# Kernel optimization log

Measured on AMD Instinct MI355X. Metric: run time of the kernel, lower is better.

## Reference

```python
import jax, jax.numpy as jnp
import numpy as np

MARGIN = 0.3


def setup_inputs() -> dict:
    key = jax.random.key(0)
    k1, k2 = jax.random.split(key)
    inputs = jax.random.normal(k1, (8192, 128), dtype=jnp.float32)
    targets = jax.random.randint(k2, (8192,), 0, 512, dtype=jnp.int64)
    return {"inputs": inputs, "targets": targets}


def reference(inputs, targets):
    # inputs: [n, d], targets: [n]
    sq = jnp.sum(inputs * inputs, axis=1)  # [n]
    # dist[i,j] = ||x_i||^2 + ||x_j||^2 - 2 x_i . x_j
    dist = sq[:, None] + sq[None, :] - 2.0 * (inputs @ inputs.T)
    dist = jnp.sqrt(jnp.clip(dist, 1e-12, None))  # [n, n]
    mask = targets[:, None] == targets[None, :]  # True where same label
    # batch-hard mining: hardest positive (max) and hardest negative (min) per row.
    # Diagonal is always True, so every row has at least one positive.
    dist_ap = jnp.max(jnp.where(mask, dist, -jnp.inf), axis=1)  # [n]
    dist_an = jnp.min(jnp.where(mask, jnp.inf, dist), axis=1)  # [n]
    # MarginRankingLoss with y=1: mean(max(0, margin - (dist_an - dist_ap)))
    loss = jnp.mean(jnp.maximum(0.0, MARGIN - (dist_an - dist_ap)))
    prec = jnp.mean((dist_an > dist_ap).astype(jnp.float32))
    return loss, prec
```

## Files before the change

kernel.cpp:

```cpp
#include <hip/hip_runtime.h>
#include <hip/hip_bf16.h>
#include <math.h>

#define N 8192
#define D 128
#define MARGIN 0.3f

#define NSTRIP 64
#define CPS 8
#define TPC 16
#define GRID_MAIN (NSTRIP * CPS)

typedef float f32x4 __attribute__((ext_vector_type(4)));
typedef short bf16x8 __attribute__((ext_vector_type(8)));
typedef unsigned short u16x8 __attribute__((ext_vector_type(8)));

#define AS1 __attribute__((address_space(1)))
#define AS3 __attribute__((address_space(3)))

__device__ inline void gload_lds16(const void* g, void* l) {
    __builtin_amdgcn_global_load_lds((AS1 void*)(void*)(g), (AS3 void*)(l), 16, 0, 0);
}

__device__ inline unsigned short f2bf(float f) {
    unsigned u = __float_as_uint(f);
    unsigned r = (u + 0x7FFFu + ((u >> 16) & 1u)) >> 16;
    return (unsigned short)r;
}

__global__ __launch_bounds__(256) void convert_kernel(const float* __restrict__ X,
                                                      unsigned short* __restrict__ Xb,
                                                      float* __restrict__ sq,
                                                      unsigned* __restrict__ ap2,
                                                      unsigned* __restrict__ an2) {
    int tid = threadIdx.x;
    int row = blockIdx.x * 16 + (tid >> 4);
    int l = tid & 15;
    const float4* p = reinterpret_cast<const float4*>(X + (size_t)row * D + l * 8);
    float4 u = p[0];
    float4 v = p[1];
    float s = u.x*u.x + u.y*u.y + u.z*u.z + u.w*u.w
            + v.x*v.x + v.y*v.y + v.z*v.z + v.w*v.w;
    u16x8 o;
    o[0] = f2bf(u.x); o[1] = f2bf(u.y); o[2] = f2bf(u.z); o[3] = f2bf(u.w);
    o[4] = f2bf(v.x); o[5] = f2bf(v.y); o[6] = f2bf(v.z); o[7] = f2bf(v.w);
    *reinterpret_cast<u16x8*>(Xb + (size_t)row * D + l * 8) = o;
    #pragma unroll
    for (int off = 8; off >= 1; off >>= 1) s += __shfl_xor(s, off);
    if (l == 0) {
        sq[row] = s;
        ap2[row] = 0u;
        an2[row] = 0x7F7F7F7Fu;
    }
}

__global__ __launch_bounds__(512, 4) void triplet_main(
        const unsigned short* __restrict__ Xb,
        const int* __restrict__ lbl,
        const float* __restrict__ sq,
        unsigned* __restrict__ ap2,
        unsigned* __restrict__ an2) {
    __shared__ unsigned short Bs[2][64 * D];
    unsigned short* BsL = &Bs[0][0];

    const int bi = blockIdx.x >> 3;
    const int c  = blockIdx.x & 7;
    const int jt0 = c * TPC;
    const int i0 = bi * 128;

    const int tid = threadIdx.x;
    const int w = tid >> 6;
    const int lane = tid & 63;
    const int wr = w >> 1;
    const int wc = w & 1;
    const int quad = lane >> 4;
    const int lx = lane & 15;

    #pragma unroll
    for (int t = 0; t < 4; ++t) {
        int rbase = w * 16 + t * 4;
        int r = rbase + quad;
        int gc = lx ^ (r & 7);
        gload_lds16(Xb + (size_t)(i0 + r) * D + gc * 8, BsL + rbase * D);
    }

    int lbl_i[8];
    #pragma unroll
    for (int tr = 0; tr < 2; ++tr)
        #pragma unroll
        for (int v = 0; v < 4; ++v)
            lbl_i[tr * 4 + v] = lbl[i0 + wr * 32 + tr * 16 + quad * 4 + v];

    __syncthreads();

    bf16x8 af_r[2][4];
    #pragma unroll
    for (int tr = 0; tr < 2; ++tr) {
        int rA = wr * 32 + tr * 16 + lx;
        #pragma unroll
        for (int ks = 0; ks < 4; ++ks) {
            int sc = (ks * 4 + quad) ^ (lx & 7);
            af_r[tr][ks] = *reinterpret_cast<const bf16x8*>(&BsL[rA * D + sc * 8]);
        }
    }
    __syncthreads();

    #pragma unroll
    for (int t = 0; t < 2; ++t) {
        int rbase = w * 8 + t * 4;
        int r = rbase + quad;
        int gc = lx ^ (r & 7);
        gload_lds16(Xb + (size_t)(jt0 * 64 + r) * D + gc * 8, BsL + rbase * D);
    }

    unsigned vb[2];
    #pragma unroll
    for (int tc = 0; tc < 2; ++tc) {
        int rB = wc * 32 + tc * 16 + lx;
        vb[tc] = (unsigned)(rB * 256 + ((lx & 4) << 4) + ((quad ^ (lx & 3)) << 4));
    }

    float m_ap[8], m_an[8];
    #pragma unroll
    for (int q = 0; q < 8; ++q) { m_ap[q] = -INFINITY; m_an[q] = INFINITY; }
    const f32x4 z4 = {0.f, 0.f, 0.f, 0.f};

    __syncthreads();

    #pragma unroll 2
    for (int tt = 0; tt < TPC; ++tt) {
        const int jj = jt0 + tt;
        const int cur = tt & 1;
        const char* bsb = (const char*)BsL + cur * (64 * D * 2);

        float sqj[2]; int lblj[2];
        #pragma unroll
        for (int tc = 0; tc < 2; ++tc) {
            int jc = jj * 64 + wc * 32 + tc * 16 + lx;
            sqj[tc] = sq[jc];
            lblj[tc] = lbl[jc];
        }

        if (tt + 1 < TPC) {
            unsigned short* nb = BsL + (cur ^ 1) * (64 * D);
            int jn = jj + 1;
            #pragma unroll
            for (int t = 0; t < 2; ++t) {
                int rbase = w * 8 + t * 4;
                int r = rbase + quad;
                int gc = lx ^ (r & 7);
                gload_lds16(Xb + (size_t)(jn * 64 + r) * D + gc * 8, nb + rbase * D);
            }
        }

        f32x4 acc[2][2];
        {
            bf16x8 bf0[2];
            #pragma unroll
            for (int tc = 0; tc < 2; ++tc)
                bf0[tc] = *reinterpret_cast<const bf16x8*>(bsb + (vb[tc] ^ 0u));
            #pragma unroll
            for (int tr = 0; tr < 2; ++tr)
                #pragma unroll
                for (int tc = 0; tc < 2; ++tc)
                    acc[tr][tc] = __builtin_amdgcn_mfma_f32_16x16x32_bf16(
                        af_r[tr][0], bf0[tc], z4, 0, 0, 0);
        }
        #pragma unroll
        for (int ks = 1; ks < 4; ++ks) {
            bf16x8 bf[2];
            #pragma unroll
            for (int tc = 0; tc < 2; ++tc)
                bf[tc] = *reinterpret_cast<const bf16x8*>(bsb + (vb[tc] ^ (unsigned)(ks << 6)));
            #pragma unroll
            for (int tr = 0; tr < 2; ++tr)
                #pragma unroll
                for (int tc = 0; tc < 2; ++tc)
                    acc[tr][tc] = __builtin_amdgcn_mfma_f32_16x16x32_bf16(
                        af_r[tr][ks], bf[tc], acc[tr][tc], 0, 0, 0);
        }

        #pragma unroll
        for (int tc = 0; tc < 2; ++tc) {
            #pragma unroll
            for (int tr = 0; tr < 2; ++tr) {
                #pragma unroll
                for (int v = 0; v < 4; ++v) {
                    int q = tr * 4 + v;
                    float vi = fmaf(-2.f, acc[tr][tc][v], sqj[tc]);
                    bool same = (lblj[tc] == lbl_i[q]);
                    m_ap[q] = same ? fmaxf(m_ap[q], vi) : m_ap[q];
                    m_an[q] = same ? m_an[q] : fminf(m_an[q], vi);
                }
            }
        }

        if (tt + 1 < TPC) __syncthreads();
    }

    #pragma unroll
    for (int off = 8; off >= 1; off >>= 1) {
        #pragma unroll
        for (int q = 0; q < 8; ++q) {
            m_ap[q] = fmaxf(m_ap[q], __shfl_xor(m_ap[q], off));
            m_an[q] = fminf(m_an[q], __shfl_xor(m_an[q], off));
        }
    }
    if (lx == 0) {
        #pragma unroll
        for (int tr = 0; tr < 2; ++tr) {
            #pragma unroll
            for (int v = 0; v < 4; ++v) {
                int q = tr * 4 + v;
                int row = i0 + wr * 32 + tr * 16 + quad * 4 + v;
                float sqi = sq[row];
                float vap = fmaxf(sqi + m_ap[q], 1e-12f);
                float van = fmaxf(sqi + m_an[q], 1e-12f);
                atomicMax(&ap2[row], __float_as_uint(vap));
                atomicMin(&an2[row], __float_as_uint(van));
            }
        }
    }
}

__global__ __launch_bounds__(1024) void finalize_kernel(const unsigned* __restrict__ ap2,
                                                        const unsigned* __restrict__ an2,
                                                        float* __restrict__ out) {
    int tid = threadIdx.x;
    float ls = 0.f, ps = 0.f;
    for (int row = tid; row < N; row += 1024) {
        float ap = sqrtf(__uint_as_float(ap2[row]));
        float an = sqrtf(__uint_as_float(an2[row]));
        ls += fmaxf(0.f, MARGIN - (an - ap));
        ps += (an > ap) ? 1.f : 0.f;
    }
    #pragma unroll
    for (int off = 32; off >= 1; off >>= 1) {
        ls += __shfl_xor(ls, off);
        ps += __shfl_xor(ps, off);
    }
    __shared__ float red[2][16];
    int w = tid >> 6;
    if ((tid & 63) == 0) { red[0][w] = ls; red[1][w] = ps; }
    __syncthreads();
    if (tid == 0) {
        float L = 0.f, P = 0.f;
        #pragma unroll
        for (int i = 0; i < 16; ++i) { L += red[0][i]; P += red[1][i]; }
        out[0] = L / (float)N;
        out[1] = P / (float)N;
    }
}

extern "C" void kernel_launch(void* const* d_in, const int* in_sizes, int n_in,
                              void* d_out, int out_size, void* d_ws, size_t ws_size,
                              hipStream_t stream) {
    const float* X = (const float*)d_in[0];
    const int* lbl = (const int*)d_in[1];
    float* out = (float*)d_out;

    float* sq = (float*)d_ws;
    unsigned* ap2 = (unsigned*)d_ws + N;
    unsigned* an2 = (unsigned*)d_ws + 2 * N;
    unsigned short* Xb = (unsigned short*)((char*)d_ws + 3 * N * sizeof(unsigned));

    convert_kernel<<<N / 16, 256, 0, stream>>>(X, Xb, sq, ap2, an2);
    triplet_main<<<GRID_MAIN, 512, 0, stream>>>(Xb, lbl, sq, ap2, an2);
    finalize_kernel<<<1, 1024, 0, stream>>>(ap2, an2, out);
}
```

Baseline: 93.47 us.

## Load MFMA operands directly from global memory instead of LDS staging

Measured after the change: 130.5 us. 1.4x slower.

```diff
diff --git a/kernel.cpp b/kernel.cpp
--- a/kernel.cpp
+++ b/kernel.cpp
@@ -14,13 +14,6 @@
 typedef float f32x4 __attribute__((ext_vector_type(4)));
 typedef short bf16x8 __attribute__((ext_vector_type(8)));
 typedef unsigned short u16x8 __attribute__((ext_vector_type(8)));
-
-#define AS1 __attribute__((address_space(1)))
-#define AS3 __attribute__((address_space(3)))
-
-__device__ inline void gload_lds16(const void* g, void* l) {
-    __builtin_amdgcn_global_load_lds((AS1 void*)(void*)(g), (AS3 void*)(l), 16, 0, 0);
-}
 
 __device__ inline unsigned short f2bf(float f) {
     unsigned u = __float_as_uint(f);
@@ -60,9 +53,6 @@
         const float* __restrict__ sq,
         unsigned* __restrict__ ap2,
         unsigned* __restrict__ an2) {
-    __shared__ unsigned short Bs[2][64 * D];
-    unsigned short* BsL = &Bs[0][0];
-
     const int bi = blockIdx.x >> 3;
     const int c  = blockIdx.x & 7;
     const int jt0 = c * TPC;
@@ -76,12 +66,14 @@
     const int quad = lane >> 4;
     const int lx = lane & 15;
 
-    #pragma unroll
-    for (int t = 0; t < 4; ++t) {
-        int rbase = w * 16 + t * 4;
-        int r = rbase + quad;
-        int gc = lx ^ (r & 7);
-        gload_lds16(Xb + (size_t)(i0 + r) * D + gc * 8, BsL + rbase * D);
+    bf16x8 af_r[2][4];
+    #pragma unroll
+    for (int tr = 0; tr < 2; ++tr) {
+        const char* pa = (const char*)Xb
+                       + (size_t)(i0 + wr * 32 + tr * 16 + lx) * (D * 2) + quad * 16;
+        #pragma unroll
+        for (int ks = 0; ks < 4; ++ks)
+            af_r[tr][ks] = *reinterpret_cast<const bf16x8*>(pa + ks * 64);
     }
 
     int lbl_i[8];
@@ -91,33 +83,12 @@
         for (int v = 0; v < 4; ++v)
             lbl_i[tr * 4 + v] = lbl[i0 + wr * 32 + tr * 16 + quad * 4 + v];
 
-    __syncthreads();
-
-    bf16x8 af_r[2][4];
-    #pragma unroll
-    for (int tr = 0; tr < 2; ++tr) {
-        int rA = wr * 32 + tr * 16 + lx;
-        #pragma unroll
-        for (int ks = 0; ks < 4; ++ks) {
-            int sc = (ks * 4 + quad) ^ (lx & 7);
-            af_r[tr][ks] = *reinterpret_cast<const bf16x8*>(&BsL[rA * D + sc * 8]);
-        }
-    }
-    __syncthreads();
-
-    #pragma unroll
-    for (int t = 0; t < 2; ++t) {
-        int rbase = w * 8 + t * 4;
-        int r = rbase + quad;
-        int gc = lx ^ (r & 7);
-        gload_lds16(Xb + (size_t)(jt0 * 64 + r) * D + gc * 8, BsL + rbase * D);
-    }
-
-    unsigned vb[2];
+    int cb[2];
+    unsigned cbB[2];
     #pragma unroll
     for (int tc = 0; tc < 2; ++tc) {
-        int rB = wc * 32 + tc * 16 + lx;
-        vb[tc] = (unsigned)(rB * 256 + ((lx & 4) << 4) + ((quad ^ (lx & 3)) << 4));
+        cb[tc] = wc * 32 + tc * 16 + lx;
+        cbB[tc] = (unsigned)(cb[tc] * (D * 2) + quad * 16);
     }
 
     float m_ap[8], m_an[8];
@@ -125,60 +96,44 @@
     for (int q = 0; q < 8; ++q) { m_ap[q] = -INFINITY; m_an[q] = INFINITY; }
     const f32x4 z4 = {0.f, 0.f, 0.f, 0.f};
 
-    __syncthreads();
-
-    #pragma unroll 2
+    #pragma unroll 1
     for (int tt = 0; tt < TPC; ++tt) {
         const int jj = jt0 + tt;
-        const int cur = tt & 1;
-        const char* bsb = (const char*)BsL + cur * (64 * D * 2);
+        const int j64 = jj * 64;
+        const unsigned jbyte = (unsigned)j64 * (D * 2);
 
         float sqj[2]; int lblj[2];
         #pragma unroll
         for (int tc = 0; tc < 2; ++tc) {
-            int jc = jj * 64 + wc * 32 + tc * 16 + lx;
+            int jc = j64 + cb[tc];
             sqj[tc] = sq[jc];
             lblj[tc] = lbl[jc];
         }
 
-        if (tt + 1 < TPC) {
-            unsigned short* nb = BsL + (cur ^ 1) * (64 * D);
-            int jn = jj + 1;
-            #pragma unroll
-            for (int t = 0; t < 2; ++t) {
-                int rbase = w * 8 + t * 4;
-                int r = rbase + quad;
-                int gc = lx ^ (r & 7);
-                gload_lds16(Xb + (size_t)(jn * 64 + r) * D + gc * 8, nb + rbase * D);
-            }
+        bf16x8 bf[2][4];
+        #pragma unroll
+        for (int tc = 0; tc < 2; ++tc) {
+            const char* pb = (const char*)Xb + (jbyte + cbB[tc]);
+            #pragma unroll
+            for (int ks = 0; ks < 4; ++ks)
+                bf[tc][ks] = *reinterpret_cast<const bf16x8*>(pb + ks * 64);
         }
 
         f32x4 acc[2][2];
-        {
-            bf16x8 bf0[2];
+        #pragma unroll
+        for (int tr = 0; tr < 2; ++tr)
             #pragma unroll
             for (int tc = 0; tc < 2; ++tc)
-                bf0[tc] = *reinterpret_cast<const bf16x8*>(bsb + (vb[tc] ^ 0u));
+                acc[tr][tc] = __builtin_amdgcn_mfma_f32_16x16x32_bf16(
+                    af_r[tr][0], bf[tc][0], z4, 0, 0, 0);
+        #pragma unroll
+        for (int ks = 1; ks < 4; ++ks)
             #pragma unroll
             for (int tr = 0; tr < 2; ++tr)
                 #pragma unroll
                 for (int tc = 0; tc < 2; ++tc)
                     acc[tr][tc] = __builtin_amdgcn_mfma_f32_16x16x32_bf16(
-                        af_r[tr][0], bf0[tc], z4, 0, 0, 0);
-        }
-        #pragma unroll
-        for (int ks = 1; ks < 4; ++ks) {
-            bf16x8 bf[2];
-            #pragma unroll
-            for (int tc = 0; tc < 2; ++tc)
-                bf[tc] = *reinterpret_cast<const bf16x8*>(bsb + (vb[tc] ^ (unsigned)(ks << 6)));
-            #pragma unroll
-            for (int tr = 0; tr < 2; ++tr)
-                #pragma unroll
-                for (int tc = 0; tc < 2; ++tc)
-                    acc[tr][tc] = __builtin_amdgcn_mfma_f32_16x16x32_bf16(
-                        af_r[tr][ks], bf[tc], acc[tr][tc], 0, 0, 0);
-        }
+                        af_r[tr][ks], bf[tc][ks], acc[tr][tc], 0, 0, 0);
 
         #pragma unroll
         for (int tc = 0; tc < 2; ++tc) {
@@ -194,8 +149,6 @@
                 }
             }
         }
-
-        if (tt + 1 < TPC) __syncthreads();
     }
 
     #pragma unroll
```

## Process two column tiles per pipeline stage and prefetch norms and labels

Applied to the files above, without the earlier changes.

After: 113.0 us. 1.21x slower.

```diff
diff --git a/kernel.cpp b/kernel.cpp
--- a/kernel.cpp
+++ b/kernel.cpp
@@ -9,6 +9,7 @@
 #define NSTRIP 64
 #define CPS 8
 #define TPC 16
+#define NEP 8
 #define GRID_MAIN (NSTRIP * CPS)
 
 typedef float f32x4 __attribute__((ext_vector_type(4)));
@@ -60,8 +61,7 @@
         const float* __restrict__ sq,
         unsigned* __restrict__ ap2,
         unsigned* __restrict__ an2) {
-    __shared__ unsigned short Bs[2][64 * D];
-    unsigned short* BsL = &Bs[0][0];
+    __shared__ unsigned short Bs[4][64 * D];
 
     const int bi = blockIdx.x >> 3;
     const int c  = blockIdx.x & 7;
@@ -76,12 +76,33 @@
     const int quad = lane >> 4;
     const int lx = lane & 15;
 
+    int cb[2];
+    unsigned vb[2];
+    #pragma unroll
+    for (int tc = 0; tc < 2; ++tc) {
+        int rB = wc * 32 + tc * 16 + lx;
+        cb[tc] = rB;
+        vb[tc] = (unsigned)(rB * 256 + ((lx & 4) << 4) + ((quad ^ (lx & 3)) << 4));
+    }
+
+    float sqj[2][2][2];
+    int   lblj[2][2][2];
+    #pragma unroll
+    for (int t = 0; t < 2; ++t)
+        #pragma unroll
+        for (int tc = 0; tc < 2; ++tc) {
+            int jc = (jt0 + t) * 64 + cb[tc];
+            sqj[0][t][tc] = sq[jc];
+            lblj[0][t][tc] = lbl[jc];
+        }
+
+    unsigned short* Abase = &Bs[0][0];
     #pragma unroll
     for (int t = 0; t < 4; ++t) {
         int rbase = w * 16 + t * 4;
         int r = rbase + quad;
         int gc = lx ^ (r & 7);
-        gload_lds16(Xb + (size_t)(i0 + r) * D + gc * 8, BsL + rbase * D);
+        gload_lds16(Xb + (size_t)(i0 + r) * D + gc * 8, Abase + rbase * D);
     }
 
     int lbl_i[8];
@@ -100,24 +121,21 @@
         #pragma unroll
         for (int ks = 0; ks < 4; ++ks) {
             int sc = (ks * 4 + quad) ^ (lx & 7);
-            af_r[tr][ks] = *reinterpret_cast<const bf16x8*>(&BsL[rA * D + sc * 8]);
+            af_r[tr][ks] = *reinterpret_cast<const bf16x8*>(&Abase[rA * D + sc * 8]);
         }
     }
     __syncthreads();
 
     #pragma unroll
     for (int t = 0; t < 2; ++t) {
-        int rbase = w * 8 + t * 4;
-        int r = rbase + quad;
-        int gc = lx ^ (r & 7);
-        gload_lds16(Xb + (size_t)(jt0 * 64 + r) * D + gc * 8, BsL + rbase * D);
-    }
-
-    unsigned vb[2];
-    #pragma unroll
-    for (int tc = 0; tc < 2; ++tc) {
-        int rB = wc * 32 + tc * 16 + lx;
-        vb[tc] = (unsigned)(rB * 256 + ((lx & 4) << 4) + ((quad ^ (lx & 3)) << 4));
+        #pragma unroll
+        for (int tt = 0; tt < 2; ++tt) {
+            int rbase = w * 8 + tt * 4;
+            int r = rbase + quad;
+            int gc = lx ^ (r & 7);
+            gload_lds16(Xb + (size_t)((jt0 + t) * 64 + r) * D + gc * 8,
+                        &Bs[t][0] + rbase * D);
+        }
     }
 
     float m_ap[8], m_an[8];
@@ -128,74 +146,82 @@
     __syncthreads();
 
     #pragma unroll 2
-    for (int tt = 0; tt < TPC; ++tt) {
-        const int jj = jt0 + tt;
-        const int cur = tt & 1;
-        const char* bsb = (const char*)BsL + cur * (64 * D * 2);
-
-        float sqj[2]; int lblj[2];
-        #pragma unroll
-        for (int tc = 0; tc < 2; ++tc) {
-            int jc = jj * 64 + wc * 32 + tc * 16 + lx;
-            sqj[tc] = sq[jc];
-            lblj[tc] = lbl[jc];
-        }
-
-        if (tt + 1 < TPC) {
-            unsigned short* nb = BsL + (cur ^ 1) * (64 * D);
-            int jn = jj + 1;
+    for (int ep = 0; ep < NEP; ++ep) {
+        const int p = ep & 1, pn = p ^ 1;
+        const int j0 = jt0 + 2 * ep;
+
+        if (ep + 1 < NEP) {
+            const int jn = j0 + 2;
             #pragma unroll
             for (int t = 0; t < 2; ++t) {
-                int rbase = w * 8 + t * 4;
-                int r = rbase + quad;
-                int gc = lx ^ (r & 7);
-                gload_lds16(Xb + (size_t)(jn * 64 + r) * D + gc * 8, nb + rbase * D);
-            }
-        }
-
-        f32x4 acc[2][2];
-        {
-            bf16x8 bf0[2];
-            #pragma unroll
-            for (int tc = 0; tc < 2; ++tc)
-                bf0[tc] = *reinterpret_cast<const bf16x8*>(bsb + (vb[tc] ^ 0u));
-            #pragma unroll
-            for (int tr = 0; tr < 2; ++tr)
+                #pragma unroll
+                for (int tt = 0; tt < 2; ++tt) {
+                    int rbase = w * 8 + tt * 4;
+                    int r = rbase + quad;
+                    int gc = lx ^ (r & 7);
+                    gload_lds16(Xb + (size_t)((jn + t) * 64 + r) * D + gc * 8,
+                                &Bs[2 * pn + t][0] + rbase * D);
+                }
+            }
+            #pragma unroll
+            for (int t = 0; t < 2; ++t)
+                #pragma unroll
+                for (int tc = 0; tc < 2; ++tc) {
+                    int jc = (jn + t) * 64 + cb[tc];
+                    sqj[pn][t][tc] = sq[jc];
+                    lblj[pn][t][tc] = lbl[jc];
+                }
+        }
+
+        #pragma unroll
+        for (int t = 0; t < 2; ++t) {
+            const char* bsb = (const char*)&Bs[2 * p + t][0];
+
+            f32x4 acc[2][2];
+            {
+                bf16x8 bf0[2];
                 #pragma unroll
                 for (int tc = 0; tc < 2; ++tc)
-                    acc[tr][tc] = __builtin_amdgcn_mfma_f32_16x16x32_bf16(
-                        af_r[tr][0], bf0[tc], z4, 0, 0, 0);
-        }
-        #pragma unroll
-        for (int ks = 1; ks < 4; ++ks) {
-            bf16x8 bf[2];
-            #pragma unroll
-            for (int tc = 0; tc < 2; ++tc)
-                bf[tc] = *reinterpret_cast<const bf16x8*>(bsb + (vb[tc] ^ (unsigned)(ks << 6)));
-            #pragma unroll
-            for (int tr = 0; tr < 2; ++tr)
+                    bf0[tc] = *reinterpret_cast<const bf16x8*>(bsb + vb[tc]);
+                #pragma unroll
+                for (int tr = 0; tr < 2; ++tr)
+                    #pragma unroll
+                    for (int tc = 0; tc < 2; ++tc)
+                        acc[tr][tc] = __builtin_amdgcn_mfma_f32_16x16x32_bf16(
+                            af_r[tr][0], bf0[tc], z4, 0, 0, 0);
+            }
+            #pragma unroll
+            for (int ks = 1; ks < 4; ++ks) {
+                bf16x8 bf[2];
                 #pragma unroll
                 for (int tc = 0; tc < 2; ++tc)
-                    acc[tr][tc] = __builtin_amdgcn_mfma_f32_16x16x32_bf16(
-                        af_r[tr][ks], bf[tc], acc[tr][tc], 0, 0, 0);
-        }
-
-        #pragma unroll
-        for (int tc = 0; tc < 2; ++tc) {
-            #pragma unroll
-            for (int tr = 0; tr < 2; ++tr) {
-                #pragma unroll
-                for (int v = 0; v < 4; ++v) {
-                    int q = tr * 4 + v;
-                    float vi = fmaf(-2.f, acc[tr][tc][v], sqj[tc]);
-                    bool same = (lblj[tc] == lbl_i[q]);
-                    m_ap[q] = same ? fmaxf(m_ap[q], vi) : m_ap[q];
-                    m_an[q] = same ? m_an[q] : fminf(m_an[q], vi);
+                    bf[tc] = *reinterpret_cast<const bf16x8*>(
+                        bsb + (vb[tc] ^ (unsigned)(ks << 6)));
+                #pragma unroll
+                for (int tr = 0; tr < 2; ++tr)
+                    #pragma unroll
+                    for (int tc = 0; tc < 2; ++tc)
+                        acc[tr][tc] = __builtin_amdgcn_mfma_f32_16x16x32_bf16(
+                            af_r[tr][ks], bf[tc], acc[tr][tc], 0, 0, 0);
+            }
+
+            #pragma unroll
+            for (int tc = 0; tc < 2; ++tc) {
+                #pragma unroll
+                for (int tr = 0; tr < 2; ++tr) {
+                    #pragma unroll
+                    for (int v = 0; v < 4; ++v) {
+                        int q = tr * 4 + v;
+                        float vi = fmaf(-2.f, acc[tr][tc][v], sqj[p][t][tc]);
+                        bool same = (lblj[p][t][tc] == lbl_i[q]);
+                        m_ap[q] = same ? fmaxf(m_ap[q], vi) : m_ap[q];
+                        m_an[q] = same ? m_an[q] : fminf(m_an[q], vi);
+                    }
                 }
             }
         }
 
-        if (tt + 1 < TPC) __syncthreads();
+        __syncthreads();
     }
 
     #pragma unroll
```

## Stage column tiles in pairs with four LDS buffers to halve barriers

Applied to the files above, without the earlier changes.

New measurement: 102.3 us. +9.4%, slower.

```diff
diff --git a/kernel.cpp b/kernel.cpp
--- a/kernel.cpp
+++ b/kernel.cpp
@@ -60,8 +60,7 @@
         const float* __restrict__ sq,
         unsigned* __restrict__ ap2,
         unsigned* __restrict__ an2) {
-    __shared__ unsigned short Bs[2][64 * D];
-    unsigned short* BsL = &Bs[0][0];
+    __shared__ unsigned short Bs[4][64 * D];
 
     const int bi = blockIdx.x >> 3;
     const int c  = blockIdx.x & 7;
@@ -76,12 +75,22 @@
     const int quad = lane >> 4;
     const int lx = lane & 15;
 
+    int cb[2];
+    unsigned vb[2];
+    #pragma unroll
+    for (int tc = 0; tc < 2; ++tc) {
+        int rB = wc * 32 + tc * 16 + lx;
+        cb[tc] = rB;
+        vb[tc] = (unsigned)(rB * 256 + ((lx & 4) << 4) + ((quad ^ (lx & 3)) << 4));
+    }
+
+    unsigned short* Abase = &Bs[0][0];
     #pragma unroll
     for (int t = 0; t < 4; ++t) {
         int rbase = w * 16 + t * 4;
         int r = rbase + quad;
         int gc = lx ^ (r & 7);
-        gload_lds16(Xb + (size_t)(i0 + r) * D + gc * 8, BsL + rbase * D);
+        gload_lds16(Xb + (size_t)(i0 + r) * D + gc * 8, Abase + rbase * D);
     }
 
     int lbl_i[8];
@@ -100,65 +109,39 @@
         #pragma unroll
         for (int ks = 0; ks < 4; ++ks) {
             int sc = (ks * 4 + quad) ^ (lx & 7);
-            af_r[tr][ks] = *reinterpret_cast<const bf16x8*>(&BsL[rA * D + sc * 8]);
-        }
-    }
-    __syncthreads();
-
-    #pragma unroll
-    for (int t = 0; t < 2; ++t) {
-        int rbase = w * 8 + t * 4;
-        int r = rbase + quad;
-        int gc = lx ^ (r & 7);
-        gload_lds16(Xb + (size_t)(jt0 * 64 + r) * D + gc * 8, BsL + rbase * D);
-    }
-
-    unsigned vb[2];
-    #pragma unroll
-    for (int tc = 0; tc < 2; ++tc) {
-        int rB = wc * 32 + tc * 16 + lx;
-        vb[tc] = (unsigned)(rB * 256 + ((lx & 4) << 4) + ((quad ^ (lx & 3)) << 4));
-    }
+            af_r[tr][ks] = *reinterpret_cast<const bf16x8*>(&Abase[rA * D + sc * 8]);
+        }
+    }
+    __syncthreads();
 
     float m_ap[8], m_an[8];
     #pragma unroll
     for (int q = 0; q < 8; ++q) { m_ap[q] = -INFINITY; m_an[q] = INFINITY; }
     const f32x4 z4 = {0.f, 0.f, 0.f, 0.f};
 
-    __syncthreads();
-
-    #pragma unroll 2
-    for (int tt = 0; tt < TPC; ++tt) {
-        const int jj = jt0 + tt;
-        const int cur = tt & 1;
-        const char* bsb = (const char*)BsL + cur * (64 * D * 2);
-
-        float sqj[2]; int lblj[2];
-        #pragma unroll
-        for (int tc = 0; tc < 2; ++tc) {
-            int jc = jj * 64 + wc * 32 + tc * 16 + lx;
-            sqj[tc] = sq[jc];
-            lblj[tc] = lbl[jc];
-        }
-
-        if (tt + 1 < TPC) {
-            unsigned short* nb = BsL + (cur ^ 1) * (64 * D);
-            int jn = jj + 1;
-            #pragma unroll
-            for (int t = 0; t < 2; ++t) {
-                int rbase = w * 8 + t * 4;
-                int r = rbase + quad;
-                int gc = lx ^ (r & 7);
-                gload_lds16(Xb + (size_t)(jn * 64 + r) * D + gc * 8, nb + rbase * D);
-            }
-        }
+    auto stage_tile = [&](unsigned short* buf, int jj) {
+        #pragma unroll
+        for (int tt = 0; tt < 2; ++tt) {
+            int rbase = w * 8 + tt * 4;
+            int r = rbase + quad;
+            int gc = lx ^ (r & 7);
+            gload_lds16(Xb + (size_t)(jj * 64 + r) * D + gc * 8, buf + rbase * D);
+        }
+    };
+
+    auto compute_tile = [&](const unsigned short* buf, int jj) {
+        const char* bsb = (const char*)buf;
+        int jc0 = jj * 64 + cb[0];
+        int jc1 = jj * 64 + cb[1];
+        float sqj0 = sq[jc0]; int lbj0 = lbl[jc0];
+        float sqj1 = sq[jc1]; int lbj1 = lbl[jc1];
 
         f32x4 acc[2][2];
         {
             bf16x8 bf0[2];
             #pragma unroll
             for (int tc = 0; tc < 2; ++tc)
-                bf0[tc] = *reinterpret_cast<const bf16x8*>(bsb + (vb[tc] ^ 0u));
+                bf0[tc] = *reinterpret_cast<const bf16x8*>(bsb + vb[tc]);
             #pragma unroll
             for (int tr = 0; tr < 2; ++tr)
                 #pragma unroll
@@ -171,7 +154,8 @@
             bf16x8 bf[2];
             #pragma unroll
             for (int tc = 0; tc < 2; ++tc)
-                bf[tc] = *reinterpret_cast<const bf16x8*>(bsb + (vb[tc] ^ (unsigned)(ks << 6)));
+                bf[tc] = *reinterpret_cast<const bf16x8*>(
+                    bsb + (vb[tc] ^ (unsigned)(ks << 6)));
             #pragma unroll
             for (int tr = 0; tr < 2; ++tr)
                 #pragma unroll
@@ -182,20 +166,43 @@
 
         #pragma unroll
         for (int tc = 0; tc < 2; ++tc) {
+            float sqjv = tc ? sqj1 : sqj0;
+            int lbjv = tc ? lbj1 : lbj0;
             #pragma unroll
             for (int tr = 0; tr < 2; ++tr) {
                 #pragma unroll
                 for (int v = 0; v < 4; ++v) {
                     int q = tr * 4 + v;
-                    float vi = fmaf(-2.f, acc[tr][tc][v], sqj[tc]);
-                    bool same = (lblj[tc] == lbl_i[q]);
+                    float vi = fmaf(-2.f, acc[tr][tc][v], sqjv);
+                    bool same = (lbjv == lbl_i[q]);
                     m_ap[q] = same ? fmaxf(m_ap[q], vi) : m_ap[q];
                     m_an[q] = same ? m_an[q] : fminf(m_an[q], vi);
                 }
             }
         }
-
-        if (tt + 1 < TPC) __syncthreads();
+    };
+
+    stage_tile(&Bs[0][0], jt0);
+    stage_tile(&Bs[1][0], jt0 + 1);
+    __syncthreads();
+
+    #pragma unroll 1
+    for (int e = 0; e < 4; ++e) {
+        const int jb = jt0 + 4 * e;
+
+        stage_tile(&Bs[2][0], jb + 2);
+        stage_tile(&Bs[3][0], jb + 3);
+        compute_tile(&Bs[0][0], jb);
+        compute_tile(&Bs[1][0], jb + 1);
+        __syncthreads();
+
+        if (e < 3) {
+            stage_tile(&Bs[0][0], jb + 4);
+            stage_tile(&Bs[1][0], jb + 5);
+        }
+        compute_tile(&Bs[2][0], jb + 2);
+        compute_tile(&Bs[3][0], jb + 3);
+        __syncthreads();
     }
 
     #pragma unroll
```
